# Kernel optimization log

Measured on AMD Instinct MI355X. Metric: run time of the kernel, lower is better.

Reference implementation:

```python
import jax, jax.numpy as jnp
import numpy as np

N, IN_DIM, OUT_DIM, HEADS = 4096, 256, 256, 8
D_HEAD = (OUT_DIM * HEADS) // HEADS  # = OUT_DIM per the torch code
HIDDEN = OUT_DIM * 4
LN_EPS = 1e-5


def setup_inputs() -> dict:
    key = jax.random.key(0)
    ks = jax.random.split(key, 8)
    s = 0.02
    return {
        "x": jax.random.normal(ks[0], (N, IN_DIM), jnp.float32),
        "Wq": jax.random.normal(ks[1], (OUT_DIM * HEADS, IN_DIM), jnp.float32) * s,
        "Wk": jax.random.normal(ks[2], (OUT_DIM * HEADS, IN_DIM), jnp.float32) * s,
        "Wv": jax.random.normal(ks[3], (OUT_DIM * HEADS, IN_DIM), jnp.float32) * s,
        "Wo": jax.random.normal(ks[4], (OUT_DIM, OUT_DIM * HEADS), jnp.float32) * s,
        "bo": jnp.zeros((OUT_DIM,), jnp.float32),
        "ln1_g": jnp.ones((IN_DIM,), jnp.float32),
        "ln1_b": jnp.zeros((IN_DIM,), jnp.float32),
        "ln2_g": jnp.ones((OUT_DIM,), jnp.float32),
        "ln2_b": jnp.zeros((OUT_DIM,), jnp.float32),
        "W1": jax.random.normal(ks[5], (HIDDEN, OUT_DIM), jnp.float32) * s,
        "b1": jnp.zeros((HIDDEN,), jnp.float32),
        "W2": jax.random.normal(ks[6], (OUT_DIM, HIDDEN), jnp.float32) * s,
        "b2": jnp.zeros((OUT_DIM,), jnp.float32),
    }


def _layernorm(x, g, b):
    mu = jnp.mean(x, axis=-1, keepdims=True)
    var = jnp.mean(jnp.square(x - mu), axis=-1, keepdims=True)
    return (x - mu) * jax.lax.rsqrt(var + LN_EPS) * g + b


def reference(x, Wq, Wk, Wv, Wo, bo, ln1_g, ln1_b, ln2_g, ln2_b, W1, b1, W2, b2):
    n = x.shape[0]
    h = _layernorm(x, ln1_g, ln1_b)
    # projections: F.linear(h, W) = h @ W.T, viewed as [N, H, d_head]
    Q = (h @ Wq.T).reshape(n, HEADS, D_HEAD)
    K = (h @ Wk.T).reshape(n, HEADS, D_HEAD)
    V = (h @ Wv.T).reshape(n, HEADS, D_HEAD)
    scores = jnp.einsum('nhd,mhd->nhm', Q, K) / jnp.sqrt(jnp.float32(D_HEAD))
    probs = jax.nn.softmax(scores, axis=-1)
    attn = jnp.einsum('nhm,mhd->nhd', probs, V).reshape(n, HEADS * D_HEAD)
    attn_out = attn @ Wo.T + bo
    x = x + attn_out  # proj_residual is Identity (in_dim == out_dim)
    h2 = _layernorm(x, ln2_g, ln2_b)
    ffn = jax.nn.gelu(h2 @ W1.T + b1, approximate=False) @ W2.T + b2
    return x + ffn
```

## Files before the change

### kernel.cpp

```cpp
#include <hip/hip_runtime.h>

typedef __attribute__((ext_vector_type(8))) short short8;
typedef __attribute__((ext_vector_type(4))) float f32x4;
typedef __attribute__((ext_vector_type(16))) float f32x16;
typedef __attribute__((ext_vector_type(8))) int i32x8;
typedef unsigned short u16;
typedef unsigned int u32;
typedef unsigned char u8;

#define DEVFN static __device__ __forceinline__

DEVFN u16 f2b(float f) {
  u32 u = __builtin_bit_cast(u32, f);
  u32 r = u + 0x7fffu + ((u >> 16) & 1u);
  return (u16)(r >> 16);
}

DEVFN float b2f(u16 b) {
  u32 u = ((u32)b) << 16;
  return __builtin_bit_cast(float, u);
}

DEVFN short8 ldfrag(const void* p) {
  return __builtin_bit_cast(short8, *(const uint4*)p);
}

#define MFMA16(a, b, c) __builtin_amdgcn_mfma_f32_16x16x32_bf16((a), (b), (c), 0, 0, 0)
#define MFMAS(a, b, c) __builtin_amdgcn_mfma_scale_f32_32x32x64_f8f6f4((a), (b), (c), 0, 0, 0, 127, 0, 127)
#define MFMASW(a, b, c) __builtin_amdgcn_mfma_scale_f32_32x32x64_f8f6f4((a), (b), (c), 0, 0, 0, 127, 0, 123)
#define EXP2(x) __builtin_amdgcn_exp2f(x)
#define CVT8(a, b, o, hi) __builtin_amdgcn_cvt_pk_fp8_f32((a), (b), (o), (hi))

DEVFN i32x8 mk8(uint4 a, uint4 b) {
  return (i32x8){(int)a.x, (int)a.y, (int)a.z, (int)a.w, (int)b.x, (int)b.y, (int)b.z, (int)b.w};
}

DEVFN void llds16(const void* g, void* l) {
  __builtin_amdgcn_global_load_lds((const __attribute__((address_space(1))) void*)g,
                                   (__attribute__((address_space(3))) void*)l, 16, 0, 0);
}

DEVFN float gelu_exact(float v) {
  return 0.5f * v * (1.0f + erff(v * 0.70710678118654752f));
}

DEVFN int sigma(int d) {
  return (d & ~24) | ((d & 8) << 1) | ((d & 16) >> 1);
}

DEVFN size_t c8off(int row, int k) {
  return (size_t)(row >> 5) * 8192 + (k >> 6) * 2048 + ((row & 31) + 32 * ((k >> 5) & 1)) * 32 + (k & 31);
}

__global__ __launch_bounds__(256) void k_prep(const float* Wq, const float* Wk, const float* Wv,
                                              const float* Wo, const float* W1, const float* W2,
                                              u8* Wq8, u8* Wk8, u8* Wv8,
                                              u16* Wob, u16* W1b, u16* W2b,
                                              const float* x, const float* g1, const float* be1,
                                              u8* h8c) {
  const int y = blockIdx.y;
  if (y < 3) {
    int i = blockIdx.x * 256 + threadIdx.x;
    if (i >= 131072) return;
    const float* s = y == 0 ? Wq : (y == 1 ? Wk : Wv);
    u8* d = y == 0 ? Wq8 : (y == 1 ? Wk8 : Wv8);
    float4 v = ((const float4*)s)[i];
    const int col = i >> 6, k = (i & 63) * 4;
    u32 q = CVT8(v.x * 16.0f, v.y * 16.0f, 0, false);
    q = CVT8(v.z * 16.0f, v.w * 16.0f, q, true);
    *(u32*)(d + c8off(col, k)) = q;
    return;
  }
  if (y < 6) {
    int i = blockIdx.x * 256 + threadIdx.x;
    const float* s;
    u16* d;
    int n4;
    switch (y) {
      case 3: s = Wo; d = Wob; n4 = 131072; break;
      case 4: s = W1; d = W1b; n4 = 65536; break;
      default: s = W2; d = W2b; n4 = 65536; break;
    }
    if (i >= n4) return;
    float4 v = ((const float4*)s)[i];
    ushort4 o = { f2b(v.x), f2b(v.y), f2b(v.z), f2b(v.w) };
    ((ushort4*)d)[i] = o;
    return;
  }
  int row = blockIdx.x * 4 + (threadIdx.x >> 6);
  int l = threadIdx.x & 63;
  const float4 v = *(const float4*)(x + (size_t)row * 256 + l * 4);
  float s = v.x + v.y + v.z + v.w;
#pragma unroll
  for (int m = 1; m < 64; m <<= 1) s += __shfl_xor(s, m);
  float mu = s * (1.0f / 256.0f);
  float dx = v.x - mu, dy = v.y - mu, dz = v.z - mu, dw = v.w - mu;
  float q = dx * dx + dy * dy + dz * dz + dw * dw;
#pragma unroll
  for (int m = 1; m < 64; m <<= 1) q += __shfl_xor(q, m);
  float r = rsqrtf(q * (1.0f / 256.0f) + 1e-5f);
  float4 gv = *(const float4*)(g1 + l * 4);
  float4 bv = *(const float4*)(be1 + l * 4);
  u32 pk = CVT8(dx * r * gv.x + bv.x, dy * r * gv.y + bv.y, 0, false);
  pk = CVT8(dz * r * gv.z + bv.z, dw * r * gv.w + bv.w, pk, true);
  *(u32*)(h8c + c8off(row, l * 4)) = pk;
}

template <int EPI>
__global__ __launch_bounds__(256, 2) void k_gemm(const u16* __restrict__ A,
                                                 const u16* __restrict__ B,
                                                 void* __restrict__ out,
                                                 const float* __restrict__ bias,
                                                 int M, int N, int K) {
  __shared__ __attribute__((aligned(16))) u16 As[128 * 32];
  __shared__ __attribute__((aligned(16))) u16 Bs[128 * 32];
  const int t = threadIdx.x;
  const int w = t >> 6, l = t & 63, g = l >> 4, c = l & 15;
  const int wr = w >> 1, wc = w & 1;
  const int bm = blockIdx.y, bn = blockIdx.x;

  f32x4 acc[4][4] = {};
  int nk = K >> 5, kk0 = 0;
  if (EPI == 4) { nk = nk / gridDim.z; kk0 = blockIdx.z * nk; }

  const int srow = t >> 2;
  const int sj = t & 3;
  const char* Abase = (const char*)A;
  const char* Bbase = (const char*)B;

  for (int kk = kk0; kk < kk0 + nk; ++kk) {
    const size_t kb = (size_t)kk * 64;
    uint4 a0 = *(const uint4*)(Abase + ((size_t)(bm * 128 + srow) * K) * 2 + kb + sj * 16);
    uint4 a1 = *(const uint4*)(Abase + ((size_t)(bm * 128 + srow + 64) * K) * 2 + kb + sj * 16);
    uint4 b0 = *(const uint4*)(Bbase + ((size_t)(bn * 128 + srow) * K) * 2 + kb + sj * 16);
    uint4 b1 = *(const uint4*)(Bbase + ((size_t)(bn * 128 + srow + 64) * K) * 2 + kb + sj * 16);
    __syncthreads();
    const int sw0 = (sj * 16) ^ (((srow >> 1) & 3) << 4);
    const int sw1 = (sj * 16) ^ ((((srow + 64) >> 1) & 3) << 4);
    *(uint4*)((char*)As + srow * 64 + sw0) = a0;
    *(uint4*)((char*)As + (srow + 64) * 64 + sw1) = a1;
    *(uint4*)((char*)Bs + srow * 64 + sw0) = b0;
    *(uint4*)((char*)Bs + (srow + 64) * 64 + sw1) = b1;
    __syncthreads();
    short8 af[4], bfr[4];
#pragma unroll
    for (int m = 0; m < 4; ++m) {
      int row = wr * 64 + m * 16 + c;
      af[m] = ldfrag((const char*)As + row * 64 + ((g * 16) ^ (((row >> 1) & 3) << 4)));
    }
#pragma unroll
    for (int n = 0; n < 4; ++n) {
      int row = wc * 64 + n * 16 + c;
      bfr[n] = ldfrag((const char*)Bs + row * 64 + ((g * 16) ^ (((row >> 1) & 3) << 4)));
    }
#pragma unroll
    for (int m = 0; m < 4; ++m)
#pragma unroll
      for (int n = 0; n < 4; ++n) acc[m][n] = MFMA16(af[m], bfr[n], acc[m][n]);
  }

  const int row0 = bm * 128 + wr * 64 + 4 * g;
  const int col0 = bn * 128 + wc * 64 + c;
#pragma unroll
  for (int m = 0; m < 4; ++m) {
#pragma unroll
    for (int n = 0; n < 4; ++n) {
      const int row = row0 + m * 16;
      const int col = col0 + n * 16;
      if (EPI == 3) {
        float bc = bias[col];
#pragma unroll
        for (int rr = 0; rr < 4; ++rr)
          ((u16*)out)[(size_t)(row + rr) * N + col] = f2b(gelu_exact(acc[m][n][rr] + bc));
      } else {
        float* po = (float*)out + (size_t)blockIdx.z * M * N;
#pragma unroll
        for (int rr = 0; rr < 4; ++rr)
          po[(size_t)(row + rr) * N + col] = acc[m][n][rr];
      }
    }
  }
}

__global__ __launch_bounds__(256, 2) void k_gemm_wo(const u16* __restrict__ part,
                                                    const float* __restrict__ ml,
                                                    const u16* __restrict__ B,
                                                    float* __restrict__ out) {
  constexpr int M = 4096, N = 256, K = 2048;
  __shared__ __attribute__((aligned(16))) u16 As[128 * 32];
  __shared__ __attribute__((aligned(16))) u16 Bs[128 * 32];
  const int t = threadIdx.x;
  const int w = t >> 6, l = t & 63, g = l >> 4, c = l & 15;
  const int wr = w >> 1, wc = w & 1;
  const int bm = blockIdx.y, bn = blockIdx.x;
  const int nk = 16, kk0 = blockIdx.z * 16;
  const int h0 = kk0 >> 3;

  const int srow = t >> 2;
  const int sj = t & 3;
  const int r0 = bm * 128 + srow, r1 = r0 + 64;

  float wgt[4];
#pragma unroll
  for (int rr = 0; rr < 2; ++rr) {
    const int row = rr ? r1 : r0;
#pragma unroll
    for (int hh = 0; hh < 2; ++hh) {
      const int h = h0 + hh;
      float l0 = ml[(0 + h) * 4096 + row];
      float l1 = ml[(8 + h) * 4096 + row];
      wgt[rr * 2 + hh] = 1.0f / (l0 + l1);
    }
  }

  f32x4 acc[4][4] = {};
  const char* Pbase = (const char*)part;
  const char* Bbase = (const char*)B;
  const size_t PSTRIDE = (size_t)4096 * 2048 * 2;

  for (int kk = kk0; kk < kk0 + nk; ++kk) {
    const int hh = (kk >> 3) & 1;
    const size_t kb = (size_t)kk * 64;
    const size_t a0off = ((size_t)r0 * K) * 2 + kb + sj * 16;
    const size_t a1off = ((size_t)r1 * K) * 2 + kb + sj * 16;
    uint4 p00 = *(const uint4*)(Pbase + a0off);
    uint4 p01 = *(const uint4*)(Pbase + PSTRIDE + a0off);
    uint4 p10 = *(const uint4*)(Pbase + a1off);
    uint4 p11 = *(const uint4*)(Pbase + PSTRIDE + a1off);
    uint4 b0 = *(const uint4*)(Bbase + ((size_t)(bn * 128 + srow) * K) * 2 + kb + sj * 16);
    uint4 b1 = *(const uint4*)(Bbase + ((size_t)(bn * 128 + srow + 64) * K) * 2 + kb + sj * 16);

    float w0 = wgt[hh], w1 = wgt[2 + hh];
    uint4 a0, a1;
    {
      const u16* x0 = (const u16*)&p00;
      const u16* x1 = (const u16*)&p01;
      u16* o = (u16*)&a0;
#pragma unroll
      for (int j = 0; j < 8; ++j) o[j] = f2b((b2f(x0[j]) + b2f(x1[j])) * w0);
      const u16* y0 = (const u16*)&p10;
      const u16* y1 = (const u16*)&p11;
      u16* o1 = (u16*)&a1;
#pragma unroll
      for (int j = 0; j < 8; ++j) o1[j] = f2b((b2f(y0[j]) + b2f(y1[j])) * w1);
    }

    __syncthreads();
    const int sw0 = (sj * 16) ^ (((srow >> 1) & 3) << 4);
    const int sw1 = (sj * 16) ^ ((((srow + 64) >> 1) & 3) << 4);
    *(uint4*)((char*)As + srow * 64 + sw0) = a0;
    *(uint4*)((char*)As + (srow + 64) * 64 + sw1) = a1;
    *(uint4*)((char*)Bs + srow * 64 + sw0) = b0;
    *(uint4*)((char*)Bs + (srow + 64) * 64 + sw1) = b1;
    __syncthreads();
    short8 af[4], bfr[4];
#pragma unroll
    for (int m = 0; m < 4; ++m) {
      int row = wr * 64 + m * 16 + c;
      af[m] = ldfrag((const char*)As + row * 64 + ((g * 16) ^ (((row >> 1) & 3) << 4)));
    }
#pragma unroll
    for (int n = 0; n < 4; ++n) {
      int row = wc * 64 + n * 16 + c;
      bfr[n] = ldfrag((const char*)Bs + row * 64 + ((g * 16) ^ (((row >> 1) & 3) << 4)));
    }
#pragma unroll
    for (int m = 0; m < 4; ++m)
#pragma unroll
      for (int n = 0; n < 4; ++n) acc[m][n] = MFMA16(af[m], bfr[n], acc[m][n]);
  }

  const int row0 = bm * 128 + wr * 64 + 4 * g;
  const int col0 = bn * 128 + wc * 64 + c;
  float* po = out + (size_t)blockIdx.z * M * N;
#pragma unroll
  for (int m = 0; m < 4; ++m)
#pragma unroll
    for (int n = 0; n < 4; ++n)
#pragma unroll
      for (int rr = 0; rr < 4; ++rr)
        po[(size_t)(row0 + m * 16 + rr) * N + col0 + n * 16] = acc[m][n][rr];
}

__global__ __launch_bounds__(256, 2) void k_gemm_qkv(const u8* __restrict__ h8c,
                                                     const u8* __restrict__ Wq8,
                                                     const u8* __restrict__ Wk8,
                                                     const u8* __restrict__ Wv8,
                                                     u8* __restrict__ Oq,
                                                     u8* __restrict__ Ok,
                                                     u8* __restrict__ Ov8) {
  __shared__ __attribute__((aligned(16))) char As[32768];
  __shared__ __attribute__((aligned(16))) char Bs[32768];
  const int t = threadIdx.x;
  const int w = t >> 6, l = t & 63;
  const int q31 = l & 31, hi = l >> 5;
  const int wr = w >> 1, wc = w & 1;
  const int sel = blockIdx.x >> 4;
  const int bn = blockIdx.x & 15;
  const int bm = blockIdx.y;
  const u8* B = sel == 0 ? Wq8 : (sel == 1 ? Wk8 : Wv8);

#pragma unroll
  for (int ii = 0; ii < 8; ++ii) {
    const int inst = w * 8 + ii;
    llds16(h8c + (size_t)bm * 32768 + inst * 1024 + l * 16, As + inst * 1024);
  }
#pragma unroll
  for (int ii = 0; ii < 8; ++ii) {
    const int inst = w * 8 + ii;
    llds16(B + (size_t)bn * 32768 + inst * 1024 + l * 16, Bs + inst * 1024);
  }
  asm volatile("s_waitcnt vmcnt(0)" ::: "memory");
  __builtin_amdgcn_s_barrier();

  f32x16 acc[2][2] = {};
#pragma unroll
  for (int ks = 0; ks < 4; ++ks) {
    i32x8 af[2], bf8[2];
#pragma unroll
    for (int m = 0; m < 2; ++m) {
      const char* p = As + ((wr * 2 + m) * 4 + ks) * 2048 + l * 32;
      af[m] = mk8(*(const uint4*)p, *(const uint4*)(p + 16));
    }
#pragma unroll
    for (int n = 0; n < 2; ++n) {
      const char* p = Bs + ((wc * 2 + n) * 4 + ks) * 2048 + l * 32;
      bf8[n] = mk8(*(const uint4*)p, *(const uint4*)(p + 16));
    }
#pragma unroll
    for (int m = 0; m < 2; ++m)
#pragma unroll
      for (int n = 0; n < 2; ++n) acc[m][n] = MFMASW(af[m], bf8[n], acc[m][n]);
  }

#pragma unroll
  for (int m = 0; m < 2; ++m) {
#pragma unroll
    for (int n = 0; n < 2; ++n) {
      const int col = bn * 128 + wc * 64 + n * 32 + q31;
      const int rbase = bm * 128 + wr * 64 + m * 32 + 4 * hi;
      const int d = col & 255, h = col >> 8;
#pragma unroll
      for (int j = 0; j < 4; ++j) {
        const int kv0 = rbase + 8 * j;
        u32 q = CVT8(acc[m][n][4 * j], acc[m][n][4 * j + 1], 0, false);
        q = CVT8(acc[m][n][4 * j + 2], acc[m][n][4 * j + 3], q, true);
        if (sel == 0) {
#pragma unroll
          for (int e = 0; e < 4; ++e)
            Oq[(size_t)(kv0 + e) * 2048 + col] = (u8)(q >> (8 * e));
        } else if (sel == 1) {
#pragma unroll
          for (int e = 0; e < 4; ++e) {
            const int kv = kv0 + e;
            Ok[(size_t)h * 1048576 + (size_t)(kv >> 5) * 8192 + (d >> 6) * 2048 +
               (((d & 31) >> 4)) * 1024 + ((kv & 31) + 32 * ((d >> 5) & 1)) * 16 + (d & 15)] =
                (u8)(q >> (8 * e));
          }
        } else {
          const int s = sigma(kv0 & 31);
          *(u32*)(Ov8 + (size_t)h * 1048576 + (size_t)(kv0 >> 6) * 16384 + (d >> 5) * 2048 +
                  ((kv0 >> 5) & 1) * 1024 + ((d & 31) + 32 * (s >> 4)) * 16 + (s & 15)) = q;
        }
      }
    }
  }
}

__global__ __launch_bounds__(256) void k_red4(const float* __restrict__ p,
                                              const float* __restrict__ bias,
                                              const float* __restrict__ resid,
                                              float* __restrict__ out) {
  int i = blockIdx.x * 256 + threadIdx.x;
  const float4* p4 = (const float4*)p;
  float4 a = p4[i], b = p4[i + 262144], c = p4[i + 524288], d = p4[i + 786432];
  float4 r = ((const float4*)resid)[i];
  float4 bb = ((const float4*)bias)[i & 63];
  float4 o;
  o.x = a.x + b.x + c.x + d.x + r.x + bb.x;
  o.y = a.y + b.y + c.y + d.y + r.y + bb.y;
  o.z = a.z + b.z + c.z + d.z + r.z + bb.z;
  o.w = a.w + b.w + c.w + d.w + r.w + bb.w;
  ((float4*)out)[i] = o;
}

__global__ __launch_bounds__(256) void k_red4ln(const float* __restrict__ p,
                                                const float* __restrict__ bias,
                                                const float* __restrict__ resid,
                                                const float* __restrict__ g,
                                                const float* __restrict__ b,
                                                float* __restrict__ x2,
                                                u16* __restrict__ out) {
  int row = blockIdx.x * 4 + (threadIdx.x >> 6);
  int l = threadIdx.x & 63;
  int i = row * 64 + l;
  const float4* p4 = (const float4*)p;
  float4 a = p4[i], bq = p4[i + 262144], cq = p4[i + 524288], dq = p4[i + 786432];
  float4 r = ((const float4*)resid)[i];
  float4 bi = ((const float4*)bias)[l];
  float4 v;
  v.x = a.x + bq.x + cq.x + dq.x + r.x + bi.x;
  v.y = a.y + bq.y + cq.y + dq.y + r.y + bi.y;
  v.z = a.z + bq.z + cq.z + dq.z + r.z + bi.z;
  v.w = a.w + bq.w + cq.w + dq.w + r.w + bi.w;
  ((float4*)x2)[i] = v;
  float s = v.x + v.y + v.z + v.w;
#pragma unroll
  for (int m = 1; m < 64; m <<= 1) s += __shfl_xor(s, m);
  float mu = s * (1.0f / 256.0f);
  float dx = v.x - mu, dy = v.y - mu, dz = v.z - mu, dw = v.w - mu;
  float q = dx * dx + dy * dy + dz * dz + dw * dw;
#pragma unroll
  for (int m = 1; m < 64; m <<= 1) q += __shfl_xor(q, m);
  float rr = rsqrtf(q * (1.0f / 256.0f) + 1e-5f);
  float4 gv = *(const float4*)(g + l * 4);
  float4 bv = *(const float4*)(b + l * 4);
  ushort4 o = { f2b(dx * rr * gv.x + bv.x), f2b(dy * rr * gv.y + bv.y),
                f2b(dz * rr * gv.z + bv.z), f2b(dw * rr * gv.w + bv.w) };
  *(ushort4*)(out + (size_t)row * 256 + l * 4) = o;
}

__global__ __launch_bounds__(256, 2) void k_attn(const u8* __restrict__ Q8,
                                                 const u8* __restrict__ K8,
                                                 const u8* __restrict__ V8,
                                                 u16* __restrict__ part,
                                                 float* __restrict__ ml) {
  __shared__ __attribute__((aligned(16))) char smem[49152];
  const int t = threadIdx.x;
  const int w = t >> 6, l = t & 63;
  const int q31 = l & 31, hi = l >> 5;
  const int head = blockIdx.x, qb = blockIdx.y, sp = blockIdx.z;
  const int cbase = sp * 64;
  const float C2 = 0.0625f * 1.44269504f;
  const float MC = 16.0f * C2;

  i32x8 qv[4];
  {
    const u8* qp = Q8 + (size_t)(qb * 128 + w * 32 + q31) * 2048 + head * 256 + hi * 32;
#pragma unroll
    for (int m = 0; m < 4; ++m)
      qv[m] = mk8(*(const uint4*)(qp + m * 64), *(const uint4*)(qp + m * 64 + 16));
  }

  f32x16 o[8] = {};
  float lsum = 0.0f;

  const u8* Kc = K8 + (size_t)head * 1048576;
  const u8* Vc = V8 + (size_t)head * 1048576;

  auto stageK = [&](int cc) {
    char* kd = smem + (cc & 1) * 8192;
    const u8* src = Kc + (size_t)(cbase + cc) * 8192;
#pragma unroll
    for (int ii = 0; ii < 2; ++ii) {
      const int inst = w * 2 + ii;
      llds16(src + inst * 1024 + l * 16, kd + inst * 1024);
    }
  };
  auto stageV = [&](int pp) {
    char* vd = smem + 16384 + (pp & 1) * 16384;
    const u8* src = Vc + (size_t)(sp * 32 + pp) * 16384;
#pragma unroll
    for (int ii = 0; ii < 4; ++ii) {
      const int inst = w * 4 + ii;
      llds16(src + inst * 1024 + l * 16, vd + inst * 1024);
    }
  };

  auto qkchunk = [&](int c, u32 pq[4]) {
    const char* kd = smem + (c & 1) * 8192;
    f32x16 s = {};
    __builtin_amdgcn_s_setprio(1);
#pragma unroll
    for (int m = 0; m < 4; ++m) {
      uint4 k0 = *(const uint4*)(kd + m * 2048 + l * 16);
      uint4 k1 = *(const uint4*)(kd + m * 2048 + 1024 + l * 16);
      s = MFMAS(mk8(k0, k1), qv[m], s);
    }
    __builtin_amdgcn_s_setprio(0);
    float p[16];
#pragma unroll
    for (int i = 0; i < 16; ++i) p[i] = EXP2(fmaf(s[i], C2, -MC));
    float r8[8];
#pragma unroll
    for (int i = 0; i < 8; ++i) r8[i] = p[i] + p[i + 8];
#pragma unroll
    for (int i = 0; i < 4; ++i) r8[i] += r8[i + 4];
    float rs = (r8[0] + r8[1]) + (r8[2] + r8[3]);
    rs += __shfl_xor(rs, 32);
    lsum += rs;
    u32 a0 = CVT8(p[0], p[1], 0, false);
    a0 = CVT8(p[2], p[3], a0, true);
    u32 a1 = CVT8(p[4], p[5], 0, false);
    a1 = CVT8(p[6], p[7], a1, true);
    u32 a2 = CVT8(p[8], p[9], 0, false);
    a2 = CVT8(p[10], p[11], a2, true);
    u32 a3 = CVT8(p[12], p[13], 0, false);
    a3 = CVT8(p[14], p[15], a3, true);
    asm("v_permlane32_swap_b32 %0, %1" : "+v"(a0), "+v"(a1));
    asm("v_permlane32_swap_b32 %0, %1" : "+v"(a2), "+v"(a3));
    pq[0] = a0; pq[1] = a1; pq[2] = a2; pq[3] = a3;
  };

  stageK(0);
  stageV(0);
  for (int cp = 0; cp < 32; ++cp) {
    const int c0 = 2 * cp;
    asm volatile("s_waitcnt vmcnt(4)" ::: "memory");
    __builtin_amdgcn_s_barrier();
    __builtin_amdgcn_sched_barrier(0);
    stageK(c0 + 1);
    u32 pe[4];
    qkchunk(c0, pe);

    asm volatile("s_waitcnt vmcnt(0)" ::: "memory");
    __builtin_amdgcn_s_barrier();
    __builtin_amdgcn_sched_barrier(0);
    if (cp < 31) {
      stageK(c0 + 2);
      stageV(cp + 1);
    }
    u32 po[4];
    qkchunk(c0 + 1, po);

    i32x8 a8 = {(int)pe[0], (int)pe[1], (int)pe[2], (int)pe[3],
                (int)po[0], (int)po[1], (int)po[2], (int)po[3]};
    const char* vd = smem + 16384 + (cp & 1) * 16384;
    __builtin_amdgcn_s_setprio(1);
#pragma unroll
    for (int dt = 0; dt < 8; ++dt) {
      uint4 v0 = *(const uint4*)(vd + dt * 2048 + l * 16);
      uint4 v1 = *(const uint4*)(vd + dt * 2048 + 1024 + l * 16);
      o[dt] = MFMAS(a8, mk8(v0, v1), o[dt]);
    }
    __builtin_amdgcn_s_setprio(0);
  }

  u16* pb = part + (size_t)sp * 4096 * 2048;
#pragma unroll
  for (int i = 0; i < 16; ++i) {
    const int r = (i & 3) + 8 * (i >> 2) + 4 * hi;
    const size_t qg = (size_t)(qb * 128 + w * 32 + r);
#pragma unroll
    for (int dt = 0; dt < 8; ++dt)
      pb[qg * 2048 + head * 256 + dt * 32 + q31] = f2b(o[dt][i]);
  }
  if (hi == 0) {
    const int qg = qb * 128 + w * 32 + q31;
    ml[(sp * 8 + head) * 4096 + qg] = lsum;
  }
}

extern "C" void kernel_launch(void* const* d_in, const int* in_sizes, int n_in,
                              void* d_out, int out_size, void* d_ws, size_t ws_size,
                              hipStream_t stream) {
  const float* x   = (const float*)d_in[0];
  const float* Wq  = (const float*)d_in[1];
  const float* Wk  = (const float*)d_in[2];
  const float* Wv  = (const float*)d_in[3];
  const float* Wo  = (const float*)d_in[4];
  const float* bo  = (const float*)d_in[5];
  const float* g1  = (const float*)d_in[6];
  const float* be1 = (const float*)d_in[7];
  const float* g2  = (const float*)d_in[8];
  const float* be2 = (const float*)d_in[9];
  const float* W1  = (const float*)d_in[10];
  const float* b1  = (const float*)d_in[11];
  const float* W2  = (const float*)d_in[12];
  const float* b2  = (const float*)d_in[13];

  char* ws = (char*)d_ws;
  size_t off = 0;
  auto alloc = [&](size_t n) {
    char* p = ws + off;
    off = (off + n + 255) & ~(size_t)255;
    return p;
  };
  u8*  h8c   = (u8*)alloc(4096 * 256);
  u8*  Wq8   = (u8*)alloc(2048 * 256);
  u8*  Wk8   = (u8*)alloc(2048 * 256);
  u8*  Wv8   = (u8*)alloc(2048 * 256);
  u16* Wob   = (u16*)alloc(256 * 2048 * 2);
  u16* W1b   = (u16*)alloc(1024 * 256 * 2);
  u16* W2b   = (u16*)alloc(256 * 1024 * 2);
  u8*  Qb8   = (u8*)alloc((size_t)4096 * 2048);
  u8*  Kb8   = (u8*)alloc((size_t)4096 * 2048);
  u8*  Vb8   = (u8*)alloc((size_t)2048 * 4096);
  u16* attnb = (u16*)alloc((size_t)2 * 4096 * 2048 * 2);
  float* mlb = (float*)alloc(16 * 4096 * 4);
  float* x2  = (float*)alloc(4096 * 256 * 4);
  u16* h2b   = (u16*)alloc(4096 * 256 * 2);
  u16* ffn1  = (u16*)alloc((size_t)4096 * 1024 * 2);
  float* pbuf = (float*)Qb8;

  k_prep<<<dim3(1024, 7), 256, 0, stream>>>(Wq, Wk, Wv, Wo, W1, W2,
                                            Wq8, Wk8, Wv8, Wob, W1b, W2b,
                                            x, g1, be1, h8c);

  k_gemm_qkv<<<dim3(48, 32), 256, 0, stream>>>(h8c, Wq8, Wk8, Wv8, Qb8, Kb8, Vb8);

  k_attn<<<dim3(8, 32, 2), 256, 0, stream>>>(Qb8, Kb8, Vb8, attnb, mlb);

  k_gemm_wo<<<dim3(2, 32, 4), 256, 0, stream>>>(attnb, mlb, Wob, pbuf);
  k_red4ln<<<1024, 256, 0, stream>>>(pbuf, bo, x, g2, be2, x2, h2b);
  k_gemm<3><<<dim3(8, 32), 256, 0, stream>>>(h2b, W1b, ffn1, b1, 4096, 1024, 256);
  k_gemm<4><<<dim3(2, 32, 4), 256, 0, stream>>>(ffn1, W2b, pbuf, nullptr, 4096, 256, 1024);
  k_red4<<<1024, 256, 0, stream>>>(pbuf, b2, x2, (float*)d_out);
}
```

Measured before the change: 151.5 us.

## Use FP8 for FFN1 GEMM and bf16 split-K partials

The FFN1 GEMM now runs in FP8: W1 and the LN2 output are quantized to fp8 in the packed c8off layout, and a new kernel loads whole 128x256 tiles into LDS and uses scaled 32x32 MFMA, replacing the bf16 templated GEMM. The split-K partial buffers for the Wo and W2 GEMMs are stored as bf16 instead of fp32, which halves their write and reduction traffic. In exchange, precision drops on the FFN input and on the partial sums.

```diff
diff --git a/kernel.cpp b/kernel.cpp
--- a/kernel.cpp
+++ b/kernel.cpp
@@ -55,7 +55,7 @@
 __global__ __launch_bounds__(256) void k_prep(const float* Wq, const float* Wk, const float* Wv,
                                               const float* Wo, const float* W1, const float* W2,
                                               u8* Wq8, u8* Wk8, u8* Wv8,
-                                              u16* Wob, u16* W1b, u16* W2b,
+                                              u16* Wob, u8* W18, u16* W2b,
                                               const float* x, const float* g1, const float* be1,
                                               u8* h8c) {
   const int y = blockIdx.y;
@@ -71,16 +71,21 @@
     *(u32*)(d + c8off(col, k)) = q;
     return;
   }
+  if (y == 4) {
+    int i = blockIdx.x * 256 + threadIdx.x;
+    if (i >= 65536) return;
+    float4 v = ((const float4*)W1)[i];
+    const int col = i >> 6, k = (i & 63) * 4;
+    u32 q = CVT8(v.x * 16.0f, v.y * 16.0f, 0, false);
+    q = CVT8(v.z * 16.0f, v.w * 16.0f, q, true);
+    *(u32*)(W18 + c8off(col, k)) = q;
+    return;
+  }
   if (y < 6) {
     int i = blockIdx.x * 256 + threadIdx.x;
-    const float* s;
-    u16* d;
-    int n4;
-    switch (y) {
-      case 3: s = Wo; d = Wob; n4 = 131072; break;
-      case 4: s = W1; d = W1b; n4 = 65536; break;
-      default: s = W2; d = W2b; n4 = 65536; break;
-    }
+    const float* s = (y == 3) ? Wo : W2;
+    u16* d = (y == 3) ? Wob : W2b;
+    int n4 = (y == 3) ? 131072 : 65536;
     if (i >= n4) return;
     float4 v = ((const float4*)s)[i];
     ushort4 o = { f2b(v.x), f2b(v.y), f2b(v.z), f2b(v.w) };
@@ -106,12 +111,10 @@
   *(u32*)(h8c + c8off(row, l * 4)) = pk;
 }
 
-template <int EPI>
-__global__ __launch_bounds__(256, 2) void k_gemm(const u16* __restrict__ A,
-                                                 const u16* __restrict__ B,
-                                                 void* __restrict__ out,
-                                                 const float* __restrict__ bias,
-                                                 int M, int N, int K) {
+__global__ __launch_bounds__(256, 2) void k_gemm_sk(const u16* __restrict__ A,
+                                                    const u16* __restrict__ B,
+                                                    u16* __restrict__ out,
+                                                    int M, int N, int K) {
   __shared__ __attribute__((aligned(16))) u16 As[128 * 32];
   __shared__ __attribute__((aligned(16))) u16 Bs[128 * 32];
   const int t = threadIdx.x;
@@ -120,8 +123,7 @@
   const int bm = blockIdx.y, bn = blockIdx.x;
 
   f32x4 acc[4][4] = {};
-  int nk = K >> 5, kk0 = 0;
-  if (EPI == 4) { nk = nk / gridDim.z; kk0 = blockIdx.z * nk; }
+  int nk = (K >> 5) / gridDim.z, kk0 = blockIdx.z * nk;
 
   const int srow = t >> 2;
   const int sj = t & 3;
@@ -161,31 +163,20 @@
 
   const int row0 = bm * 128 + wr * 64 + 4 * g;
   const int col0 = bn * 128 + wc * 64 + c;
-#pragma unroll
-  for (int m = 0; m < 4; ++m) {
-#pragma unroll
-    for (int n = 0; n < 4; ++n) {
-      const int row = row0 + m * 16;
-      const int col = col0 + n * 16;
-      if (EPI == 3) {
-        float bc = bias[col];
-#pragma unroll
-        for (int rr = 0; rr < 4; ++rr)
-          ((u16*)out)[(size_t)(row + rr) * N + col] = f2b(gelu_exact(acc[m][n][rr] + bc));
-      } else {
-        float* po = (float*)out + (size_t)blockIdx.z * M * N;
-#pragma unroll
-        for (int rr = 0; rr < 4; ++rr)
-          po[(size_t)(row + rr) * N + col] = acc[m][n][rr];
-      }
-    }
-  }
+  u16* po = out + (size_t)blockIdx.z * M * N;
+#pragma unroll
+  for (int m = 0; m < 4; ++m)
+#pragma unroll
+    for (int n = 0; n < 4; ++n)
+#pragma unroll
+      for (int rr = 0; rr < 4; ++rr)
+        po[(size_t)(row0 + m * 16 + rr) * N + col0 + n * 16] = f2b(acc[m][n][rr]);
 }
 
 __global__ __launch_bounds__(256, 2) void k_gemm_wo(const u16* __restrict__ part,
                                                     const float* __restrict__ ml,
                                                     const u16* __restrict__ B,
-                                                    float* __restrict__ out) {
+                                                    u16* __restrict__ out) {
   constexpr int M = 4096, N = 256, K = 2048;
   __shared__ __attribute__((aligned(16))) u16 As[128 * 32];
   __shared__ __attribute__((aligned(16))) u16 Bs[128 * 32];
@@ -272,14 +263,14 @@
 
   const int row0 = bm * 128 + wr * 64 + 4 * g;
   const int col0 = bn * 128 + wc * 64 + c;
-  float* po = out + (size_t)blockIdx.z * M * N;
+  u16* po = out + (size_t)blockIdx.z * M * N;
 #pragma unroll
   for (int m = 0; m < 4; ++m)
 #pragma unroll
     for (int n = 0; n < 4; ++n)
 #pragma unroll
       for (int rr = 0; rr < 4; ++rr)
-        po[(size_t)(row0 + m * 16 + rr) * N + col0 + n * 16] = acc[m][n][rr];
+        po[(size_t)(row0 + m * 16 + rr) * N + col0 + n * 16] = f2b(acc[m][n][rr]);
 }
 
 __global__ __launch_bounds__(256, 2) void k_gemm_qkv(const u8* __restrict__ h8c,
@@ -367,42 +358,110 @@
   }
 }
 
-__global__ __launch_bounds__(256) void k_red4(const float* __restrict__ p,
+__global__ __launch_bounds__(256, 2) void k_gemm_ffn1(const u8* __restrict__ A8,
+                                                      const u8* __restrict__ B8,
+                                                      const float* __restrict__ bias,
+                                                      u16* __restrict__ out) {
+  __shared__ __attribute__((aligned(16))) char As[32768];
+  __shared__ __attribute__((aligned(16))) char Bs[32768];
+  const int t = threadIdx.x;
+  const int w = t >> 6, l = t & 63;
+  const int q31 = l & 31, hi = l >> 5;
+  const int wr = w >> 1, wc = w & 1;
+  const int bn = blockIdx.x;
+  const int bm = blockIdx.y;
+
+#pragma unroll
+  for (int ii = 0; ii < 8; ++ii) {
+    const int inst = w * 8 + ii;
+    llds16(A8 + (size_t)bm * 32768 + inst * 1024 + l * 16, As + inst * 1024);
+  }
+#pragma unroll
+  for (int ii = 0; ii < 8; ++ii) {
+    const int inst = w * 8 + ii;
+    llds16(B8 + (size_t)bn * 32768 + inst * 1024 + l * 16, Bs + inst * 1024);
+  }
+  asm volatile("s_waitcnt vmcnt(0)" ::: "memory");
+  __builtin_amdgcn_s_barrier();
+
+  f32x16 acc[2][2] = {};
+#pragma unroll
+  for (int ks = 0; ks < 4; ++ks) {
+    i32x8 af[2], bf8[2];
+#pragma unroll
+    for (int m = 0; m < 2; ++m) {
+      const char* p = As + ((wr * 2 + m) * 4 + ks) * 2048 + l * 32;
+      af[m] = mk8(*(const uint4*)p, *(const uint4*)(p + 16));
+    }
+#pragma unroll
+    for (int n = 0; n < 2; ++n) {
+      const char* p = Bs + ((wc * 2 + n) * 4 + ks) * 2048 + l * 32;
+      bf8[n] = mk8(*(const uint4*)p, *(const uint4*)(p + 16));
+    }
+#pragma unroll
+    for (int m = 0; m < 2; ++m)
+#pragma unroll
+      for (int n = 0; n < 2; ++n) acc[m][n] = MFMASW(af[m], bf8[n], acc[m][n]);
+  }
+
+#pragma unroll
+  for (int m = 0; m < 2; ++m) {
+#pragma unroll
+    for (int n = 0; n < 2; ++n) {
+      const int col = bn * 128 + wc * 64 + n * 32 + q31;
+      const int rbase = bm * 128 + wr * 64 + m * 32 + 4 * hi;
+      const float bc = bias[col];
+#pragma unroll
+      for (int j = 0; j < 4; ++j) {
+        const int r0j = rbase + 8 * j;
+#pragma unroll
+        for (int e = 0; e < 4; ++e)
+          out[(size_t)(r0j + e) * 1024 + col] = f2b(gelu_exact(acc[m][n][4 * j + e] + bc));
+      }
+    }
+  }
+}
+
+__global__ __launch_bounds__(256) void k_red4(const u16* __restrict__ p,
                                               const float* __restrict__ bias,
                                               const float* __restrict__ resid,
                                               float* __restrict__ out) {
   int i = blockIdx.x * 256 + threadIdx.x;
-  const float4* p4 = (const float4*)p;
-  float4 a = p4[i], b = p4[i + 262144], c = p4[i + 524288], d = p4[i + 786432];
+  ushort4 a = *(const ushort4*)(p + (size_t)i * 4);
+  ushort4 b = *(const ushort4*)(p + 1048576 * 1 + (size_t)i * 4);
+  ushort4 c = *(const ushort4*)(p + 1048576 * 2 + (size_t)i * 4);
+  ushort4 d = *(const ushort4*)(p + 1048576 * 3 + (size_t)i * 4);
   float4 r = ((const float4*)resid)[i];
   float4 bb = ((const float4*)bias)[i & 63];
   float4 o;
-  o.x = a.x + b.x + c.x + d.x + r.x + bb.x;
-  o.y = a.y + b.y + c.y + d.y + r.y + bb.y;
-  o.z = a.z + b.z + c.z + d.z + r.z + bb.z;
-  o.w = a.w + b.w + c.w + d.w + r.w + bb.w;
+  o.x = b2f(a.x) + b2f(b.x) + b2f(c.x) + b2f(d.x) + r.x + bb.x;
+  o.y = b2f(a.y) + b2f(b.y) + b2f(c.y) + b2f(d.y) + r.y + bb.y;
+  o.z = b2f(a.z) + b2f(b.z) + b2f(c.z) + b2f(d.z) + r.z + bb.z;
+  o.w = b2f(a.w) + b2f(b.w) + b2f(c.w) + b2f(d.w) + r.w + bb.w;
   ((float4*)out)[i] = o;
 }
 
-__global__ __launch_bounds__(256) void k_red4ln(const float* __restrict__ p,
+__global__ __launch_bounds__(256) void k_red4ln(const u16* __restrict__ p,
                                                 const float* __restrict__ bias,
                                                 const float* __restrict__ resid,
                                                 const float* __restrict__ g,
                                                 const float* __restrict__ b,
                                                 float* __restrict__ x2,
-                                                u16* __restrict__ out) {
+                                                u8* __restrict__ h28) {
   int row = blockIdx.x * 4 + (threadIdx.x >> 6);
   int l = threadIdx.x & 63;
   int i = row * 64 + l;
-  const float4* p4 = (const float4*)p;
-  float4 a = p4[i], bq = p4[i + 262144], cq = p4[i + 524288], dq = p4[i + 786432];
+  ushort4 a = *(const ushort4*)(p + (size_t)i * 4);
+  ushort4 bq = *(const ushort4*)(p + 1048576 * 1 + (size_t)i * 4);
+  ushort4 cq = *(const ushort4*)(p + 1048576 * 2 + (size_t)i * 4);
+  ushort4 dq = *(const ushort4*)(p + 1048576 * 3 + (size_t)i * 4);
   float4 r = ((const float4*)resid)[i];
   float4 bi = ((const float4*)bias)[l];
   float4 v;
-  v.x = a.x + bq.x + cq.x + dq.x + r.x + bi.x;
-  v.y = a.y + bq.y + cq.y + dq.y + r.y + bi.y;
-  v.z = a.z + bq.z + cq.z + dq.z + r.z + bi.z;
-  v.w = a.w + bq.w + cq.w + dq.w + r.w + bi.w;
+  v.x = b2f(a.x) + b2f(bq.x) + b2f(cq.x) + b2f(dq.x) + r.x + bi.x;
+  v.y = b2f(a.y) + b2f(bq.y) + b2f(cq.y) + b2f(dq.y) + r.y + bi.y;
+  v.z = b2f(a.z) + b2f(bq.z) + b2f(cq.z) + b2f(dq.z) + r.z + bi.z;
+  v.w = b2f(a.w) + b2f(bq.w) + b2f(cq.w) + b2f(dq.w) + r.w + bi.w;
   ((float4*)x2)[i] = v;
   float s = v.x + v.y + v.z + v.w;
 #pragma unroll
@@ -415,9 +474,9 @@
   float rr = rsqrtf(q * (1.0f / 256.0f) + 1e-5f);
   float4 gv = *(const float4*)(g + l * 4);
   float4 bv = *(const float4*)(b + l * 4);
-  ushort4 o = { f2b(dx * rr * gv.x + bv.x), f2b(dy * rr * gv.y + bv.y),
-                f2b(dz * rr * gv.z + bv.z), f2b(dw * rr * gv.w + bv.w) };
-  *(ushort4*)(out + (size_t)row * 256 + l * 4) = o;
+  u32 pk = CVT8(dx * rr * gv.x + bv.x, dy * rr * gv.y + bv.y, 0, false);
+  pk = CVT8(dz * rr * gv.z + bv.z, dw * rr * gv.w + bv.w, pk, true);
+  *(u32*)(h28 + c8off(row, l * 4)) = pk;
 }
 
 __global__ __launch_bounds__(256, 2) void k_attn(const u8* __restrict__ Q8,
@@ -581,7 +640,7 @@
   u8*  Wk8   = (u8*)alloc(2048 * 256);
   u8*  Wv8   = (u8*)alloc(2048 * 256);
   u16* Wob   = (u16*)alloc(256 * 2048 * 2);
-  u16* W1b   = (u16*)alloc(1024 * 256 * 2);
+  u8*  W18   = (u8*)alloc(1024 * 256);
   u16* W2b   = (u16*)alloc(256 * 1024 * 2);
   u8*  Qb8   = (u8*)alloc((size_t)4096 * 2048);
   u8*  Kb8   = (u8*)alloc((size_t)4096 * 2048);
@@ -589,12 +648,12 @@
   u16* attnb = (u16*)alloc((size_t)2 * 4096 * 2048 * 2);
   float* mlb = (float*)alloc(16 * 4096 * 4);
   float* x2  = (float*)alloc(4096 * 256 * 4);
-  u16* h2b   = (u16*)alloc(4096 * 256 * 2);
+  u8*  h28   = (u8*)alloc(4096 * 256);
   u16* ffn1  = (u16*)alloc((size_t)4096 * 1024 * 2);
-  float* pbuf = (float*)Qb8;
+  u16* pbuf  = (u16*)Qb8;
 
   k_prep<<<dim3(1024, 7), 256, 0, stream>>>(Wq, Wk, Wv, Wo, W1, W2,
-                                            Wq8, Wk8, Wv8, Wob, W1b, W2b,
+                                            Wq8, Wk8, Wv8, Wob, W18, W2b,
                                             x, g1, be1, h8c);
 
   k_gemm_qkv<<<dim3(48, 32), 256, 0, stream>>>(h8c, Wq8, Wk8, Wv8, Qb8, Kb8, Vb8);
@@ -602,8 +661,8 @@
   k_attn<<<dim3(8, 32, 2), 256, 0, stream>>>(Qb8, Kb8, Vb8, attnb, mlb);
 
   k_gemm_wo<<<dim3(2, 32, 4), 256, 0, stream>>>(attnb, mlb, Wob, pbuf);
-  k_red4ln<<<1024, 256, 0, stream>>>(pbuf, bo, x, g2, be2, x2, h2b);
-  k_gemm<3><<<dim3(8, 32), 256, 0, stream>>>(h2b, W1b, ffn1, b1, 4096, 1024, 256);
-  k_gemm<4><<<dim3(2, 32, 4), 256, 0, stream>>>(ffn1, W2b, pbuf, nullptr, 4096, 256, 1024);
+  k_red4ln<<<1024, 256, 0, stream>>>(pbuf, bo, x, g2, be2, x2, h28);
+  k_gemm_ffn1<<<dim3(8, 32), 256, 0, stream>>>(h28, W18, b1, ffn1);
+  k_gemm_sk<<<dim3(2, 32, 4), 256, 0, stream>>>(ffn1, W2b, pbuf, 4096, 256, 1024);
   k_red4<<<1024, 256, 0, stream>>>(pbuf, b2, x2, (float*)d_out);
 }
```

Result: faster. 144.9 us (-4.3%).
